# Performance work log

Hardware: AMD Instinct MI355X
Metric: run time of the kernel (lower is better)

Reference implementation:

```python
import jax, jax.numpy as jnp
import numpy as np

TEMPERATURE = 0.5  # init temperature; attn_drop=0.0 so dropout is identity


def setup_inputs() -> dict:
    key = jax.random.key(0)
    k1, k2, k3 = jax.random.split(key, 3)
    B, H, N, D = 4, 8, 2048, 64
    q = jax.random.normal(k1, (B, H, N, D), dtype=jnp.float32)
    k = jax.random.normal(k2, (B, H, N, D), dtype=jnp.float32)
    v = jax.random.normal(k3, (B, H, N, D), dtype=jnp.float32)
    scale = jnp.asarray(D ** -0.5, dtype=jnp.float32)
    return {"q": q, "k": k, "v": v, "scale": scale}


def reference(q, k, v, scale):
    # logits: [B,H,N,N]
    logits = jnp.einsum("bhqd,bhkd->bhqk", q, k) * scale
    # first softmax acts as a soft mask over keys
    soft_mask = jax.nn.softmax(logits / TEMPERATURE, axis=-1)
    # second softmax over masked logits (elementwise product, NOT matmul)
    attn = jax.nn.softmax(logits * soft_mask, axis=-1)
    # dropout with p=0.0 is identity
    out = jnp.einsum("bhqk,bhkd->bhqd", attn, v)
    return out
```

## Files before the change

kernel.cpp:

```cpp
#include <hip/hip_runtime.h>


typedef _Float16 f16;
typedef f16 f16x8 __attribute__((ext_vector_type(8)));
typedef float f32x4 __attribute__((ext_vector_type(4)));

#define MFMA(a, b, c) __builtin_amdgcn_mfma_f32_16x16x32_f16((a), (b), (c), 0, 0, 0)
#define EXP2(x) __builtin_amdgcn_exp2f(x)

#define N_CTX 2048
#define DH 64
#define KT 64
#define NKT (N_CTX / KT)
#define ROWS 128
#define QS 72

#define C2  2.885390081777927f
#define L2E 1.442695040888963f

__device__ inline unsigned pk(float a, float b) {
    typedef __fp16 fp16x2_t __attribute__((ext_vector_type(2)));
    union { fp16x2_t v; unsigned u; } x;
    x.v = __builtin_amdgcn_cvt_pkrtz(a, b);
    return x.u;
}

__global__ __launch_bounds__(512, 4)
void stk_attn_mfma(const float* __restrict__ qg, const float* __restrict__ kg,
                   const float* __restrict__ vglob, const float* __restrict__ sg,
                   float* __restrict__ og) {
    __shared__ f16 Qs[ROWS * QS];
    __shared__ f16 Ks[2][KT * QS];
    __shared__ f16 Vt[DH * KT];
    __shared__ f16 Ps[8][16 * KT];

    const int tid  = threadIdx.x;
    const int wv   = tid >> 6;
    const int lane = tid & 63;
    const int l15  = lane & 15;
    const int q4   = lane >> 4;
    const int vp   = tid & 31;
    const int vgr  = tid >> 5;
    const int bh   = blockIdx.x & 31;
    const int q0   = (blockIdx.x >> 5) * ROWS;
    const float scale = sg[0];

    const float* qb = qg + (size_t)bh * N_CTX * DH;
    const float* kb = kg + (size_t)bh * N_CTX * DH;
    const float* vb = vglob + (size_t)bh * N_CTX * DH;
    float*       ob = og + (size_t)bh * N_CTX * DH;

    #pragma unroll
    for (int it = 0; it < 4; ++it) {
        int idx = it * 512 + tid;
        int row = idx >> 4, c4 = idx & 15;
        float4 v = *(const float4*)&qb[((size_t)(q0 + row)) * DH + c4 * 4];
        *(uint2*)&Qs[row * QS + c4 * 4] =
            make_uint2(pk(v.x * scale, v.y * scale), pk(v.z * scale, v.w * scale));
    }
    __syncthreads();

    f16x8 aq[2];
    #pragma unroll
    for (int kc = 0; kc < 2; ++kc)
        aq[kc] = *(const f16x8*)&Qs[(wv * 16 + l15) * QS + kc * 32 + q4 * 8];

    float s1[4] = {0, 0, 0, 0};
    float4 kr[2];
    #pragma unroll
    for (int it = 0; it < 2; ++it) {
        int idx = it * 512 + tid;
        kr[it] = *(const float4*)&kb[((size_t)(idx >> 4)) * DH + (idx & 15) * 4];
    }
    #pragma unroll
    for (int it = 0; it < 2; ++it) {
        int idx = it * 512 + tid;
        *(uint2*)&Ks[0][(idx >> 4) * QS + (idx & 15) * 4] =
            make_uint2(pk(kr[it].x, kr[it].y), pk(kr[it].z, kr[it].w));
    }
    #pragma unroll
    for (int it = 0; it < 2; ++it) {
        int idx = it * 512 + tid;
        kr[it] = *(const float4*)&kb[((size_t)KT + (idx >> 4)) * DH + (idx & 15) * 4];
    }
    __syncthreads();

    for (int kt = 0; kt < NKT; ++kt) {
        const int cur = kt & 1, nxt = cur ^ 1;
        #pragma unroll
        for (int it = 0; it < 2; ++it) {
            int idx = it * 512 + tid;
            *(uint2*)&Ks[nxt][(idx >> 4) * QS + (idx & 15) * 4] =
                make_uint2(pk(kr[it].x, kr[it].y), pk(kr[it].z, kr[it].w));
        }
        {
            int tn = (kt + 2 < NKT) ? kt + 2 : NKT - 1;
            #pragma unroll
            for (int it = 0; it < 2; ++it) {
                int idx = it * 512 + tid;
                kr[it] = *(const float4*)&kb[((size_t)tn * KT + (idx >> 4)) * DH + (idx & 15) * 4];
            }
        }
        #pragma unroll
        for (int kgi = 0; kgi < 4; ++kgi) {
            f16x8 b0 = *(const f16x8*)&Ks[cur][(kgi * 16 + l15) * QS + 0 * 32 + q4 * 8];
            f16x8 b1 = *(const f16x8*)&Ks[cur][(kgi * 16 + l15) * QS + 1 * 32 + q4 * 8];
            f32x4 acc = {0.f, 0.f, 0.f, 0.f};
            acc = MFMA(aq[0], b0, acc);
            acc = MFMA(aq[1], b1, acc);
            #pragma unroll
            for (int r = 0; r < 4; ++r)
                s1[r] += EXP2(acc[r] * C2);
        }
        __syncthreads();
    }
    float inv1[4];
    #pragma unroll
    for (int s = 0; s < 4; ++s) {
        float v = s1[s];
        v += __shfl_xor(v, 1, 64);
        v += __shfl_xor(v, 2, 64);
        v += __shfl_xor(v, 4, 64);
        v += __shfl_xor(v, 8, 64);
        inv1[s] = L2E / v;
    }

    float l2[4] = {0, 0, 0, 0};
    f32x4 O[4];
    #pragma unroll
    for (int dt = 0; dt < 4; ++dt) O[dt] = (f32x4){0.f, 0.f, 0.f, 0.f};

    float4 vr[2];
    #pragma unroll
    for (int it = 0; it < 2; ++it) {
        int idx = it * 512 + tid;
        kr[it] = *(const float4*)&kb[((size_t)(idx >> 4)) * DH + (idx & 15) * 4];
    }
    #pragma unroll
    for (int it = 0; it < 2; ++it) {
        int idx = it * 512 + tid;
        *(uint2*)&Ks[0][(idx >> 4) * QS + (idx & 15) * 4] =
            make_uint2(pk(kr[it].x, kr[it].y), pk(kr[it].z, kr[it].w));
    }
    {
        const float* vs = vb + ((size_t)2 * vp) * DH + vgr * 4;
        vr[0] = *(const float4*)(vs);
        vr[1] = *(const float4*)(vs + DH);
    }
    #pragma unroll
    for (int it = 0; it < 2; ++it) {
        int idx = it * 512 + tid;
        kr[it] = *(const float4*)&kb[((size_t)KT + (idx >> 4)) * DH + (idx & 15) * 4];
    }
    __syncthreads();

    for (int kt = 0; kt < NKT; ++kt) {
        const int cur = kt & 1, nxt = cur ^ 1;
        #pragma unroll
        for (int j = 0; j < 4; ++j) {
            int d = vgr * 4 + j;
            float a0 = ((const float*)&vr[0])[j];
            float a1 = ((const float*)&vr[1])[j];
            *(unsigned*)&Vt[d * KT + ((2 * vp) ^ (8 * (d & 7)))] = pk(a0, a1);
        }
        #pragma unroll
        for (int it = 0; it < 2; ++it) {
            int idx = it * 512 + tid;
            *(uint2*)&Ks[nxt][(idx >> 4) * QS + (idx & 15) * 4] =
                make_uint2(pk(kr[it].x, kr[it].y), pk(kr[it].z, kr[it].w));
        }
        #pragma unroll
        for (int kgi = 0; kgi < 4; ++kgi) {
            f16x8 b0 = *(const f16x8*)&Ks[cur][(kgi * 16 + l15) * QS + 0 * 32 + q4 * 8];
            f16x8 b1 = *(const f16x8*)&Ks[cur][(kgi * 16 + l15) * QS + 1 * 32 + q4 * 8];
            f32x4 acc = {0.f, 0.f, 0.f, 0.f};
            acc = MFMA(aq[0], b0, acc);
            acc = MFMA(aq[1], b1, acc);
            #pragma unroll
            for (int r = 0; r < 4; ++r) {
                float L  = acc[r];
                float e1 = EXP2(L * C2);
                float e2 = EXP2((L * e1) * inv1[r]);
                l2[r] += e2;
                int lrow = q4 * 4 + r;
                int col  = kgi * 16 + l15;
                Ps[wv][lrow * KT + (col ^ ((lrow & 7) * 8))] = (f16)e2;
            }
        }
        {
            int tv = (kt + 1 < NKT) ? kt + 1 : NKT - 1;
            int tk = (kt + 2 < NKT) ? kt + 2 : NKT - 1;
            const float* vs = vb + ((size_t)tv * KT + 2 * vp) * DH + vgr * 4;
            vr[0] = *(const float4*)(vs);
            vr[1] = *(const float4*)(vs + DH);
            #pragma unroll
            for (int it = 0; it < 2; ++it) {
                int idx = it * 512 + tid;
                kr[it] = *(const float4*)&kb[((size_t)tk * KT + (idx >> 4)) * DH + (idx & 15) * 4];
            }
        }
        __syncthreads();
        #pragma unroll
        for (int kc = 0; kc < 2; ++kc) {
            int kbase = kc * 32 + q4 * 8;
            f16x8 ap = *(const f16x8*)&Ps[wv][l15 * KT + (kbase ^ ((l15 & 7) * 8))];
            #pragma unroll
            for (int dt = 0; dt < 4; ++dt) {
                f16x8 bv = *(const f16x8*)&Vt[(dt * 16 + l15) * KT + (kbase ^ ((l15 & 7) * 8))];
                O[dt] = MFMA(ap, bv, O[dt]);
            }
        }
        __syncthreads();
    }

    float invl2[4];
    #pragma unroll
    for (int s = 0; s < 4; ++s) {
        float v = l2[s];
        v += __shfl_xor(v, 1, 64);
        v += __shfl_xor(v, 2, 64);
        v += __shfl_xor(v, 4, 64);
        v += __shfl_xor(v, 8, 64);
        invl2[s] = 1.0f / v;
    }
    #pragma unroll
    for (int dt = 0; dt < 4; ++dt)
        #pragma unroll
        for (int r = 0; r < 4; ++r) {
            int row = q0 + wv * 16 + q4 * 4 + r;
            ob[(size_t)row * DH + dt * 16 + l15] = O[dt][r] * invl2[r];
        }
}

extern "C" void kernel_launch(void* const* d_in, const int* in_sizes, int n_in,
                              void* d_out, int out_size, void* d_ws, size_t ws_size,
                              hipStream_t stream) {
    const float* q = (const float*)d_in[0];
    const float* k = (const float*)d_in[1];
    const float* v = (const float*)d_in[2];
    const float* s = (const float*)d_in[3];
    float* out = (float*)d_out;
    dim3 grid(32 * 16);
    stk_attn_mfma<<<grid, 512, 0, stream>>>(q, k, v, s, out);
}
```

Measured before the change: 173.9 us.

## Double-buffer V tile to drop a barrier and reswizzle P tile

Double-buffers the transposed V tile in shared memory so the next tile is written while the current one is read. This lets the mid-iteration __syncthreads in the second pass be removed, leaving one barrier per key tile. The V prefetch now loads two tiles ahead, matching K. The per-wave P scratch also gets a new XOR swizzle meant to reduce LDS bank conflicts. The cost is an extra 8 KB of shared memory per block.

New measurement: 175.9 us. About the same (+1.1%).

```diff
diff --git a/kernel.cpp b/kernel.cpp
--- a/kernel.cpp
+++ b/kernel.cpp
@@ -18,6 +18,8 @@
 #define C2  2.885390081777927f
 #define L2E 1.442695040888963f
 
+#define PS_S(lrow) (16 * ((lrow) >> 2) + 8 * ((lrow) & 1))
+
 __device__ inline unsigned pk(float a, float b) {
     typedef __fp16 fp16x2_t __attribute__((ext_vector_type(2)));
     union { fp16x2_t v; unsigned u; } x;
@@ -31,7 +33,7 @@
                    float* __restrict__ og) {
     __shared__ f16 Qs[ROWS * QS];
     __shared__ f16 Ks[2][KT * QS];
-    __shared__ f16 Vt[DH * KT];
+    __shared__ f16 Vt[2][DH * KT];
     __shared__ f16 Ps[8][16 * KT];
 
     const int tid  = threadIdx.x;
@@ -146,6 +148,15 @@
         const float* vs = vb + ((size_t)2 * vp) * DH + vgr * 4;
         vr[0] = *(const float4*)(vs);
         vr[1] = *(const float4*)(vs + DH);
+        #pragma unroll
+        for (int j = 0; j < 4; ++j) {
+            int d = vgr * 4 + j;
+            *(unsigned*)&Vt[0][d * KT + ((2 * vp) ^ (8 * (d & 7)))] =
+                pk(((const float*)&vr[0])[j], ((const float*)&vr[1])[j]);
+        }
+        const float* vs1 = vb + ((size_t)KT + 2 * vp) * DH + vgr * 4;
+        vr[0] = *(const float4*)(vs1);
+        vr[1] = *(const float4*)(vs1 + DH);
     }
     #pragma unroll
     for (int it = 0; it < 2; ++it) {
@@ -156,18 +167,17 @@
 
     for (int kt = 0; kt < NKT; ++kt) {
         const int cur = kt & 1, nxt = cur ^ 1;
-        #pragma unroll
-        for (int j = 0; j < 4; ++j) {
-            int d = vgr * 4 + j;
-            float a0 = ((const float*)&vr[0])[j];
-            float a1 = ((const float*)&vr[1])[j];
-            *(unsigned*)&Vt[d * KT + ((2 * vp) ^ (8 * (d & 7)))] = pk(a0, a1);
-        }
         #pragma unroll
         for (int it = 0; it < 2; ++it) {
             int idx = it * 512 + tid;
             *(uint2*)&Ks[nxt][(idx >> 4) * QS + (idx & 15) * 4] =
                 make_uint2(pk(kr[it].x, kr[it].y), pk(kr[it].z, kr[it].w));
+        }
+        #pragma unroll
+        for (int j = 0; j < 4; ++j) {
+            int d = vgr * 4 + j;
+            *(unsigned*)&Vt[nxt][d * KT + ((2 * vp) ^ (8 * (d & 7)))] =
+                pk(((const float*)&vr[0])[j], ((const float*)&vr[1])[j]);
         }
         #pragma unroll
         for (int kgi = 0; kgi < 4; ++kgi) {
@@ -184,29 +194,29 @@
                 l2[r] += e2;
                 int lrow = q4 * 4 + r;
                 int col  = kgi * 16 + l15;
-                Ps[wv][lrow * KT + (col ^ ((lrow & 7) * 8))] = (f16)e2;
+                Ps[wv][lrow * KT + (col ^ PS_S(lrow))] = (f16)e2;
             }
         }
         {
-            int tv = (kt + 1 < NKT) ? kt + 1 : NKT - 1;
-            int tk = (kt + 2 < NKT) ? kt + 2 : NKT - 1;
-            const float* vs = vb + ((size_t)tv * KT + 2 * vp) * DH + vgr * 4;
+            int tn = (kt + 2 < NKT) ? kt + 2 : NKT - 1;
+            #pragma unroll
+            for (int it = 0; it < 2; ++it) {
+                int idx = it * 512 + tid;
+                kr[it] = *(const float4*)&kb[((size_t)tn * KT + (idx >> 4)) * DH + (idx & 15) * 4];
+            }
+            const float* vs = vb + ((size_t)tn * KT + 2 * vp) * DH + vgr * 4;
             vr[0] = *(const float4*)(vs);
             vr[1] = *(const float4*)(vs + DH);
-            #pragma unroll
-            for (int it = 0; it < 2; ++it) {
-                int idx = it * 512 + tid;
-                kr[it] = *(const float4*)&kb[((size_t)tk * KT + (idx >> 4)) * DH + (idx & 15) * 4];
-            }
-        }
-        __syncthreads();
+        }
         #pragma unroll
         for (int kc = 0; kc < 2; ++kc) {
-            int kbase = kc * 32 + q4 * 8;
-            f16x8 ap = *(const f16x8*)&Ps[wv][l15 * KT + (kbase ^ ((l15 & 7) * 8))];
+            int kbase = (kc * 32 + q4 * 8) ^ PS_S(l15);
+            f16x8 ap = *(const f16x8*)&Ps[wv][l15 * KT + kbase];
+            int kbv = kc * 32 + q4 * 8;
             #pragma unroll
             for (int dt = 0; dt < 4; ++dt) {
-                f16x8 bv = *(const f16x8*)&Vt[(dt * 16 + l15) * KT + (kbase ^ ((l15 & 7) * 8))];
+                int d = dt * 16 + l15;
+                f16x8 bv = *(const f16x8*)&Vt[cur][d * KT + (kbv ^ (8 * (d & 7)))];
                 O[dt] = MFMA(ap, bv, O[dt]);
             }
         }
```
